# Performance work log

Measured on AMD Instinct MI355X. Metric: run time of the kernel, lower is better.

## Reference

```python
import jax, jax.numpy as jnp
import numpy as np

NEG_SLOPE = 0.2


def _gat_layer(x, src, dst, W, att_s, att_d, bias):
    # x: [N, F_in]; W: [F_in, H*C]; att_s/att_d: [H, C]; bias: [H*C]
    N = x.shape[0]
    H, C = att_s.shape
    h = (x @ W).reshape(N, H, C)                      # projected features [N,H,C]
    a_src = jnp.einsum('nhc,hc->nh', h, att_s)        # [N,H] per-node src logits
    a_dst = jnp.einsum('nhc,hc->nh', h, att_d)        # [N,H]
    e = a_src[src] + a_dst[dst]                       # [E,H] edge logits
    e = jnp.where(e > 0, e, NEG_SLOPE * e)            # leaky_relu
    # scatter-softmax over incoming edges of each destination node
    m = jax.ops.segment_max(e, dst, num_segments=N)   # [N,H]
    ex = jnp.exp(e - m[dst])                          # [E,H]
    denom = jax.ops.segment_sum(ex, dst, num_segments=N)  # [N,H]
    alpha = ex / denom[dst]                           # [E,H]
    # scatter-add aggregation of weighted source features
    msg = h[src] * alpha[:, :, None]                  # [E,H,C]
    out = jax.ops.segment_sum(msg, dst, num_segments=N)   # [N,H,C]
    return out.reshape(N, H * C) + bias


def _with_self_loops(edge_index, N):
    loop = jnp.arange(N, dtype=edge_index.dtype)
    src = jnp.concatenate([edge_index[0], loop])
    dst = jnp.concatenate([edge_index[1], loop])
    return src, dst


def setup_inputs() -> dict:
    key = jax.random.key(0)
    ks = jax.random.split(key, 10)
    N, E = 50000, 800000
    F_in, C1, H1, F_out = 128, 64, 4, 128
    x = jax.random.normal(ks[0], (N, F_in), dtype=jnp.float32)
    edge_index = jax.random.randint(ks[1], (2, E), 0, N, dtype=jnp.int64)
    s1 = 1.0 / np.sqrt(F_in)
    W1 = jax.random.normal(ks[2], (F_in, H1 * C1), dtype=jnp.float32) * s1
    att_src1 = jax.random.normal(ks[3], (H1, C1), dtype=jnp.float32) * 0.1
    att_dst1 = jax.random.normal(ks[4], (H1, C1), dtype=jnp.float32) * 0.1
    bias1 = jnp.zeros((H1 * C1,), dtype=jnp.float32)
    s2 = 1.0 / np.sqrt(H1 * C1)
    W2 = jax.random.normal(ks[5], (H1 * C1, F_out), dtype=jnp.float32) * s2
    att_src2 = jax.random.normal(ks[6], (1, F_out), dtype=jnp.float32) * 0.1
    att_dst2 = jax.random.normal(ks[7], (1, F_out), dtype=jnp.float32) * 0.1
    bias2 = jnp.zeros((F_out,), dtype=jnp.float32)
    return {"x": x, "edge_index": edge_index,
            "W1": W1, "att_src1": att_src1, "att_dst1": att_dst1, "bias1": bias1,
            "W2": W2, "att_src2": att_src2, "att_dst2": att_dst2, "bias2": bias2}


def reference(x, edge_index, W1, att_src1, att_dst1, bias1,
              W2, att_src2, att_dst2, bias2):
    N = x.shape[0]
    src, dst = _with_self_loops(edge_index, N)
    h1 = _gat_layer(x, src, dst, W1, att_src1, att_dst1, bias1)
    h1 = jax.nn.elu(h1)
    out = _gat_layer(h1, src, dst, W2, att_src2, att_dst2, bias2)
    return out
```

## Files before the change

kernel.cpp:

```cpp
#include <hip/hip_runtime.h>

#define NN 50000
#define NE 800000

constexpr int H1 = 4, F1 = 128, HC1 = 256;
constexpr int HC2 = 128;
constexpr int GM1 = (NN + 63) / 64;
constexpr int GE  = (NE + 255) / 256;

typedef unsigned short u16;
typedef unsigned int u32;
typedef __attribute__((ext_vector_type(8))) short bf16x8;
typedef __attribute__((ext_vector_type(4))) float f32x4;

__device__ __forceinline__ float bf2f(u16 h) {
    return __uint_as_float(((u32)h) << 16);
}
__device__ __forceinline__ u16 f2bf(float f) {
    u32 u = __float_as_uint(f);
    u32 r = (u + 0x7fffu + ((u >> 16) & 1u)) >> 16;
    return (u16)r;
}

__device__ __forceinline__ int ld_edge(const int* e32, const long long* e64, int is64, long long idx) {
    return is64 ? (int)e64[idx] : e32[idx];
}

__global__ __launch_bounds__(256) void k_prep(
    const float* __restrict__ x, const float* __restrict__ W1, const float* __restrict__ W2,
    u16* __restrict__ xb, u16* __restrict__ wp1, u16* __restrict__ wp2,
    int* __restrict__ deg, const int* __restrict__ e32, int* __restrict__ flag)
{
    const int b = blockIdx.x, tid = threadIdx.x;
    if (b < 3125) {
        int i = b * 256 + tid;
        const float4* p = (const float4*)x + (size_t)i * 2;
        float4 a = p[0], c = p[1];
        ushort4 o0, o1;
        o0.x = f2bf(a.x); o0.y = f2bf(a.y); o0.z = f2bf(a.z); o0.w = f2bf(a.w);
        o1.x = f2bf(c.x); o1.y = f2bf(c.y); o1.z = f2bf(c.z); o1.w = f2bf(c.w);
        ((ushort4*)xb)[(size_t)i * 2] = o0;
        ((ushort4*)xb)[(size_t)i * 2 + 1] = o1;
    } else if (b < 3253) {
        int o = (b - 3125) * 256 + tid;
        int j = o & 7, lk = (o >> 3) & 3, nn = (o >> 5) & 255, kc = o >> 13;
        int k = kc * 32 + lk * 8 + j;
        wp1[o] = f2bf(W1[(size_t)k * HC1 + nn]);
    } else if (b < 3381) {
        int o = (b - 3253) * 256 + tid;
        int j = o & 7, lk = (o >> 3) & 3, nn = (o >> 5) & 127, kc = o >> 12;
        int k = kc * 32 + lk * 8 + j;
        wp2[o] = f2bf(W2[(size_t)k * HC2 + nn]);
    } else {
        int i = (b - 3381) * 256 + tid;
        if (i < NN) deg[i] = 0;
        if (b == 3381 && tid == 0) {
            int z = 1;
            for (int t = 0; t < 16; t++)
                if (e32[2 * t + 1] != 0) z = 0;
            *flag = z;
        }
    }
}

__global__ void k_count(const int* __restrict__ e32, const long long* __restrict__ e64,
                        const int* __restrict__ flag, int* __restrict__ deg) {
    int e = blockIdx.x * blockDim.x + threadIdx.x;
    if (e >= NE) return;
    int is64 = *flag;
    int dst = ld_edge(e32, e64, is64, (long long)NE + e);
    atomicAdd(&deg[dst], 1);
}

__global__ __launch_bounds__(256) void k_part(const int* __restrict__ deg, int* __restrict__ bsum) {
    int i = blockIdx.x * 256 + threadIdx.x;
    int v = (i < NN) ? deg[i] : 0;
    #pragma unroll
    for (int off = 1; off < 64; off <<= 1) v += __shfl_xor(v, off);
    __shared__ int ws[4];
    if ((threadIdx.x & 63) == 0) ws[threadIdx.x >> 6] = v;
    __syncthreads();
    if (threadIdx.x == 0) bsum[blockIdx.x] = ws[0] + ws[1] + ws[2] + ws[3];
}

__global__ __launch_bounds__(256) void k_scanb(const int* __restrict__ bsum, int* __restrict__ boff,
                                               int* __restrict__ row_ptr, int NB) {
    const int tid = threadIdx.x;
    const int lane = tid & 63, wv = tid >> 6;
    int v = (tid < NB) ? bsum[tid] : 0;
    int x = v;
    #pragma unroll
    for (int off = 1; off < 64; off <<= 1) {
        int t = __shfl_up(x, off);
        if (lane >= off) x += t;
    }
    __shared__ int wsum[4], woff[4];
    if (lane == 63) wsum[wv] = x;
    __syncthreads();
    if (tid == 0) {
        int run = 0;
        #pragma unroll
        for (int j = 0; j < 4; j++) { woff[j] = run; run += wsum[j]; }
        row_ptr[NN] = run;
    }
    __syncthreads();
    if (tid < NB) boff[tid] = x - v + woff[wv];
}

__global__ __launch_bounds__(256) void k_addb(const int* __restrict__ deg, const int* __restrict__ boff,
                                              int* __restrict__ row_ptr, int* __restrict__ cursor) {
    const int tid = threadIdx.x;
    const int lane = tid & 63, wv = tid >> 6;
    int i = blockIdx.x * 256 + tid;
    int v = (i < NN) ? deg[i] : 0;
    int x = v;
    #pragma unroll
    for (int off = 1; off < 64; off <<= 1) {
        int t = __shfl_up(x, off);
        if (lane >= off) x += t;
    }
    __shared__ int wsum[4], woff[4];
    if (lane == 63) wsum[wv] = x;
    __syncthreads();
    if (tid == 0) {
        int run = 0;
        #pragma unroll
        for (int j = 0; j < 4; j++) { woff[j] = run; run += wsum[j]; }
    }
    __syncthreads();
    int excl = x - v + woff[wv] + boff[blockIdx.x];
    if (i < NN) { row_ptr[i] = excl; cursor[i] = excl; }
}

__global__ void k_fill(const int* __restrict__ e32, const long long* __restrict__ e64,
                       const int* __restrict__ flag, int* __restrict__ cursor, int* __restrict__ col) {
    int e = blockIdx.x * blockDim.x + threadIdx.x;
    if (e >= NE) return;
    int is64 = *flag;
    int src = ld_edge(e32, e64, is64, e);
    int dst = ld_edge(e32, e64, is64, (long long)NE + e);
    int pos = atomicAdd(&cursor[dst], 1);
    col[pos] = src;
}

template <int K, int NOUT, int HEADS, int TPB>
__device__ __forceinline__ void gemm_body(
    int bid, const u16* __restrict__ Ab, const u16* __restrict__ Wp,
    const float* __restrict__ atts, const float* __restrict__ attd,
    u16* __restrict__ Hout, float* __restrict__ as_out, float* __restrict__ ad_out, int M)
{
    constexpr int BM = 64, BK = 32;
    constexpr int NK = K / BK;
    constexpr int C = NOUT / HEADS;
    constexpr int LDA = 40;
    __shared__ __align__(16) u16 As[2][BM * LDA];
    __shared__ float red_s[BM * HEADS];
    __shared__ float red_d[BM * HEADS];

    const int tid = threadIdx.x;
    const int w = tid >> 6;
    const int l = tid & 63;
    const int l15 = l & 15, lk = l >> 4;
    const int row0 = bid * BM;
    const int col0 = w * 64;

    for (int i = tid; i < BM * HEADS; i += TPB) { red_s[i] = 0.f; red_d[i] = 0.f; }

    f32x4 acc[4][4];
    #pragma unroll
    for (int rt = 0; rt < 4; rt++)
        #pragma unroll
        for (int nt = 0; nt < 4; nt++)
            acc[rt][nt] = (f32x4){0.f, 0.f, 0.f, 0.f};

    auto stage = [&](int kc, int b) {
        #pragma unroll
        for (int i = tid; i < BM * 4; i += TPB) {
            int r = i >> 2, c = (i & 3) * 8;
            int gr = row0 + r;
            bf16x8 v = {0, 0, 0, 0, 0, 0, 0, 0};
            if (gr < M) v = *(const bf16x8*)(Ab + (size_t)gr * K + kc * BK + c);
            *(bf16x8*)&As[b][r * LDA + c] = v;
        }
    };
    auto loadB = [&](int kc, bf16x8* bf) {
        #pragma unroll
        for (int nt = 0; nt < 4; nt++)
            bf[nt] = *(const bf16x8*)(Wp + (((size_t)kc * NOUT + col0 + nt * 16 + l15) * 4 + lk) * 8);
    };

    bf16x8 bcur[4];
    loadB(0, bcur);
    stage(0, 0);
    for (int kc = 0; kc < NK; ++kc) {
        __syncthreads();
        bf16x8 afr[4];
        #pragma unroll
        for (int rt = 0; rt < 4; rt++)
            afr[rt] = *(const bf16x8*)&As[kc & 1][(rt * 16 + l15) * LDA + lk * 8];
        bf16x8 bnext[4];
        if (kc + 1 < NK) {
            loadB(kc + 1, bnext);
            stage(kc + 1, (kc + 1) & 1);
        }
        #pragma unroll
        for (int rt = 0; rt < 4; rt++)
            #pragma unroll
            for (int nt = 0; nt < 4; nt++)
                acc[rt][nt] = __builtin_amdgcn_mfma_f32_16x16x32_bf16(afr[rt], bcur[nt], acc[rt][nt], 0, 0, 0);
        if (kc + 1 < NK) {
            #pragma unroll
            for (int nt = 0; nt < 4; nt++) bcur[nt] = bnext[nt];
        }
    }

    #pragma unroll
    for (int rt = 0; rt < 4; rt++) {
        #pragma unroll
        for (int t = 0; t < 4; t++) {
            int gr = row0 + rt * 16 + lk * 4 + t;
            if (gr < M) {
                #pragma unroll
                for (int nt = 0; nt < 4; nt++)
                    Hout[(size_t)gr * NOUT + col0 + nt * 16 + l15] = f2bf(acc[rt][nt][t]);
            }
        }
    }

    float avs[4], avd[4];
    #pragma unroll
    for (int nt = 0; nt < 4; nt++) {
        int gc = col0 + nt * 16 + l15;
        avs[nt] = atts[gc];
        avd[nt] = attd[gc];
    }
    const int headw = col0 / C;
    #pragma unroll
    for (int rt = 0; rt < 4; rt++) {
        #pragma unroll
        for (int t = 0; t < 4; t++) {
            float ps = 0.f, pd = 0.f;
            #pragma unroll
            for (int nt = 0; nt < 4; nt++) {
                ps = fmaf(acc[rt][nt][t], avs[nt], ps);
                pd = fmaf(acc[rt][nt][t], avd[nt], pd);
            }
            ps += __shfl_xor(ps, 1); ps += __shfl_xor(ps, 2);
            ps += __shfl_xor(ps, 4); ps += __shfl_xor(ps, 8);
            pd += __shfl_xor(pd, 1); pd += __shfl_xor(pd, 2);
            pd += __shfl_xor(pd, 4); pd += __shfl_xor(pd, 8);
            if (l15 == 0) {
                int row = rt * 16 + lk * 4 + t;
                atomicAdd(&red_s[row * HEADS + headw], ps);
                atomicAdd(&red_d[row * HEADS + headw], pd);
            }
        }
    }
    __syncthreads();
    for (int i = tid; i < BM * HEADS; i += TPB) {
        int gr = row0 + i / HEADS;
        if (gr < M) {
            as_out[(size_t)gr * HEADS + i % HEADS] = red_s[i];
            ad_out[(size_t)gr * HEADS + i % HEADS] = red_d[i];
        }
    }
}

template <int K, int NOUT, int HEADS, int TPB>
__global__ __launch_bounds__(TPB) void k_gemm_mfma(
    const u16* __restrict__ Ab, const u16* __restrict__ Wp,
    const float* __restrict__ atts, const float* __restrict__ attd,
    u16* __restrict__ Hout, float* __restrict__ as_out, float* __restrict__ ad_out, int M)
{
    gemm_body<K, NOUT, HEADS, TPB>(blockIdx.x, Ab, Wp, atts, attd, Hout, as_out, ad_out, M);
}

__global__ __launch_bounds__(256) void k_agg1(
    const int* __restrict__ row_ptr, const int* __restrict__ col,
    const u16* __restrict__ Hb, const float* __restrict__ as_, const float* __restrict__ ad_,
    const float* __restrict__ bias, u16* __restrict__ outp)
{
    __shared__ int    s_src[4][64];
    __shared__ float4 s_p[4][64];
    int n = blockIdx.x * 4 + (threadIdx.x >> 6);
    const int lane = threadIdx.x & 63;
    const int wv = threadIdx.x >> 6;
    const int half = lane >> 5, l32 = lane & 31;
    const int head8 = l32 >> 3;
    float4 ad4 = *(const float4*)(ad_ + (size_t)n * 4);
    int beg = row_ptr[n];
    int cnt = row_ptr[n + 1] - beg + 1;
    float4 sp = make_float4(0.f, 0.f, 0.f, 0.f);
    float a0 = 0.f, a1 = 0.f, a2 = 0.f, a3 = 0.f;
    float a4 = 0.f, a5 = 0.f, a6 = 0.f, a7 = 0.f;
    for (int c = 0; c < cnt; c += 64) {
        int idx = c + lane;
        int srcl = n;
        float4 p4 = make_float4(0.f, 0.f, 0.f, 0.f);
        if (idx < cnt) {
            srcl = (idx == 0) ? n : col[beg + idx - 1];
            float4 aa = *(const float4*)(as_ + (size_t)srcl * 4);
            float e;
            e = aa.x + ad4.x; e = e > 0.f ? e : 0.2f * e; p4.x = __expf(e);
            e = aa.y + ad4.y; e = e > 0.f ? e : 0.2f * e; p4.y = __expf(e);
            e = aa.z + ad4.z; e = e > 0.f ? e : 0.2f * e; p4.z = __expf(e);
            e = aa.w + ad4.w; e = e > 0.f ? e : 0.2f * e; p4.w = __expf(e);
        }
        sp.x += p4.x; sp.y += p4.y; sp.z += p4.z; sp.w += p4.w;
        s_src[wv][lane] = srcl;
        s_p[wv][lane] = p4;
        int jmax = min(64, cnt - c);
        #pragma unroll 4
        for (int j = 0; j < jmax; j += 2) {
            int jj = j + half;
            int srcj = s_src[wv][jj];
            float pj = ((const float*)&s_p[wv][jj])[head8];
            bf16x8 hv = *(const bf16x8*)(Hb + (size_t)srcj * HC1 + l32 * 8);
            a0 = fmaf(pj, bf2f((u16)hv[0]), a0);
            a1 = fmaf(pj, bf2f((u16)hv[1]), a1);
            a2 = fmaf(pj, bf2f((u16)hv[2]), a2);
            a3 = fmaf(pj, bf2f((u16)hv[3]), a3);
            a4 = fmaf(pj, bf2f((u16)hv[4]), a4);
            a5 = fmaf(pj, bf2f((u16)hv[5]), a5);
            a6 = fmaf(pj, bf2f((u16)hv[6]), a6);
            a7 = fmaf(pj, bf2f((u16)hv[7]), a7);
        }
    }
    a0 += __shfl_xor(a0, 32); a1 += __shfl_xor(a1, 32);
    a2 += __shfl_xor(a2, 32); a3 += __shfl_xor(a3, 32);
    a4 += __shfl_xor(a4, 32); a5 += __shfl_xor(a5, 32);
    a6 += __shfl_xor(a6, 32); a7 += __shfl_xor(a7, 32);
    #pragma unroll
    for (int off = 1; off < 64; off <<= 1) {
        sp.x += __shfl_xor(sp.x, off);
        sp.y += __shfl_xor(sp.y, off);
        sp.z += __shfl_xor(sp.z, off);
        sp.w += __shfl_xor(sp.w, off);
    }
    if (lane < 32) {
        float s = head8 < 2 ? (head8 == 0 ? sp.x : sp.y) : (head8 == 2 ? sp.z : sp.w);
        float inv = 1.f / s;
        int ch0 = l32 * 8;
        float4 bv0 = *(const float4*)(bias + ch0);
        float4 bv1 = *(const float4*)(bias + ch0 + 4);
        float o0 = a0 * inv + bv0.x, o1 = a1 * inv + bv0.y;
        float o2 = a2 * inv + bv0.z, o3 = a3 * inv + bv0.w;
        float o4 = a4 * inv + bv1.x, o5 = a5 * inv + bv1.y;
        float o6 = a6 * inv + bv1.z, o7 = a7 * inv + bv1.w;
        o0 = o0 > 0.f ? o0 : __expf(o0) - 1.f;
        o1 = o1 > 0.f ? o1 : __expf(o1) - 1.f;
        o2 = o2 > 0.f ? o2 : __expf(o2) - 1.f;
        o3 = o3 > 0.f ? o3 : __expf(o3) - 1.f;
        o4 = o4 > 0.f ? o4 : __expf(o4) - 1.f;
        o5 = o5 > 0.f ? o5 : __expf(o5) - 1.f;
        o6 = o6 > 0.f ? o6 : __expf(o6) - 1.f;
        o7 = o7 > 0.f ? o7 : __expf(o7) - 1.f;
        bf16x8 ob;
        ob[0] = (short)f2bf(o0); ob[1] = (short)f2bf(o1);
        ob[2] = (short)f2bf(o2); ob[3] = (short)f2bf(o3);
        ob[4] = (short)f2bf(o4); ob[5] = (short)f2bf(o5);
        ob[6] = (short)f2bf(o6); ob[7] = (short)f2bf(o7);
        *(bf16x8*)(outp + (size_t)n * HC1 + ch0) = ob;
    }
}

__global__ __launch_bounds__(256) void k_agg2(
    const int* __restrict__ row_ptr, const int* __restrict__ col,
    const u16* __restrict__ Hb, const float* __restrict__ as_, const float* __restrict__ ad_,
    const float* __restrict__ bias, float* __restrict__ outp)
{
    __shared__ int   s_src[4][64];
    __shared__ float s_p[4][64];
    int n = blockIdx.x * 4 + (threadIdx.x >> 6);
    const int lane = threadIdx.x & 63;
    const int wv = threadIdx.x >> 6;
    const int half = lane >> 5, l32 = lane & 31;
    float ad0 = ad_[n];
    int beg = row_ptr[n];
    int cnt = row_ptr[n + 1] - beg + 1;
    float sp = 0.f;
    float a0 = 0.f, a1 = 0.f, a2 = 0.f, a3 = 0.f;
    for (int c = 0; c < cnt; c += 64) {
        int idx = c + lane;
        int srcl = n;
        float p = 0.f;
        if (idx < cnt) {
            srcl = (idx == 0) ? n : col[beg + idx - 1];
            float e = as_[srcl] + ad0;
            e = e > 0.f ? e : 0.2f * e;
            p = __expf(e);
        }
        sp += p;
        s_src[wv][lane] = srcl;
        s_p[wv][lane] = p;
        int jmax = min(64, cnt - c);
        #pragma unroll 4
        for (int j = 0; j < jmax; j += 2) {
            int jj = j + half;
            int srcj = s_src[wv][jj];
            float pj = s_p[wv][jj];
            ushort4 hv = *(const ushort4*)(Hb + (size_t)srcj * HC2 + l32 * 4);
            a0 = fmaf(pj, bf2f(hv.x), a0);
            a1 = fmaf(pj, bf2f(hv.y), a1);
            a2 = fmaf(pj, bf2f(hv.z), a2);
            a3 = fmaf(pj, bf2f(hv.w), a3);
        }
    }
    a0 += __shfl_xor(a0, 32); a1 += __shfl_xor(a1, 32);
    a2 += __shfl_xor(a2, 32); a3 += __shfl_xor(a3, 32);
    #pragma unroll
    for (int off = 1; off < 64; off <<= 1) sp += __shfl_xor(sp, off);
    if (lane < 32) {
        float inv = 1.f / sp;
        int ch0 = l32 * 4;
        float4 bv = *(const float4*)(bias + ch0);
        float4 o;
        o.x = a0 * inv + bv.x;
        o.y = a1 * inv + bv.y;
        o.z = a2 * inv + bv.z;
        o.w = a3 * inv + bv.w;
        *(float4*)(outp + (size_t)n * HC2 + ch0) = o;
    }
}

extern "C" void kernel_launch(void* const* d_in, const int* in_sizes, int n_in,
                              void* d_out, int out_size, void* d_ws, size_t ws_size,
                              hipStream_t stream) {
    const float* x   = (const float*)d_in[0];
    const int*       e32 = (const int*)d_in[1];
    const long long* e64 = (const long long*)d_in[1];
    const float* W1  = (const float*)d_in[2];
    const float* as1w = (const float*)d_in[3];
    const float* ad1w = (const float*)d_in[4];
    const float* b1  = (const float*)d_in[5];
    const float* W2  = (const float*)d_in[6];
    const float* as2w = (const float*)d_in[7];
    const float* ad2w = (const float*)d_in[8];
    const float* b2  = (const float*)d_in[9];
    float* out = (float*)d_out;

    char* w = (char*)d_ws;
    auto carve = [&](size_t bytes) -> void* {
        void* p = (void*)w;
        w += (bytes + 255) & ~(size_t)255;
        return p;
    };
    int*   flag    = (int*)carve(4);
    int*   row_ptr = (int*)carve((NN + 1) * sizeof(int));
    int*   cursor  = (int*)carve(NN * sizeof(int));
    int*   col     = (int*)carve(NE * sizeof(int));
    int*   bsum    = (int*)carve(256 * sizeof(int));
    int*   boff    = (int*)carve(256 * sizeof(int));
    float* as1     = (float*)carve((size_t)NN * H1 * sizeof(float));
    float* ad1     = (float*)carve((size_t)NN * H1 * sizeof(float));
    float* as2     = (float*)carve((size_t)NN * sizeof(float));
    float* ad2     = (float*)carve((size_t)NN * sizeof(float));
    u16*   xb      = (u16*)carve((size_t)NN * F1 * sizeof(u16));
    u16*   h1b     = (u16*)carve((size_t)NN * HC1 * sizeof(u16));
    u16*   h2in    = (u16*)carve((size_t)NN * HC1 * sizeof(u16));
    u16*   h2b     = (u16*)carve((size_t)NN * HC2 * sizeof(u16));
    u16*   wp1     = (u16*)carve((size_t)F1 * HC1 * sizeof(u16));
    u16*   wp2     = (u16*)carve((size_t)HC1 * HC2 * sizeof(u16));

    const int TPB = 256;
    const int gN  = (NN + TPB - 1) / TPB;
    const int gAgg = NN / 4;

    k_prep<<<3125 + 128 + 128 + 196, 256, 0, stream>>>(x, W1, W2, xb, wp1, wp2, cursor, e32, flag);

    k_count<<<GE, TPB, 0, stream>>>(e32, e64, flag, cursor);
    k_part<<<gN, TPB, 0, stream>>>(cursor, bsum);
    k_scanb<<<1, 256, 0, stream>>>(bsum, boff, row_ptr, gN);
    k_addb<<<gN, TPB, 0, stream>>>(cursor, boff, row_ptr, cursor);
    k_fill<<<GE, TPB, 0, stream>>>(e32, e64, flag, cursor, col);

    k_gemm_mfma<F1, HC1, H1, 256><<<GM1, 256, 0, stream>>>(xb, wp1, as1w, ad1w, h1b, as1, ad1, NN);
    k_agg1<<<gAgg, TPB, 0, stream>>>(row_ptr, col, h1b, as1, ad1, b1, h2in);

    k_gemm_mfma<HC1, HC2, 1, 128><<<GM1, 128, 0, stream>>>(h2in, wp2, as2w, ad2w, h2b, as2, ad2, NN);
    k_agg2<<<gAgg, TPB, 0, stream>>>(row_ptr, col, h2b, as2, ad2, b2, out);
}
```

Measured before the change: 237.3 us.

## Fuse degree counting into prep kernel and remap agg1 to one edge per wave

Degree counting moves into the prep kernel as extra blocks, and the deg array is now zeroed with a memset before launch, which removes one kernel launch. Each count block recomputes the int32/int64 edge-format check inline. Layer-1 aggregation changes its lane mapping: all 64 lanes now process one edge per step and each lane loads 4 bf16 channels, where before each half-wave handled a separate edge with 8 channels. This drops the cross-half shuffle reduction, but each lane issues narrower loads and the inner loop runs twice as many iterations.

```diff
diff --git a/kernel.cpp b/kernel.cpp
--- a/kernel.cpp
+++ b/kernel.cpp
@@ -29,7 +29,8 @@
 __global__ __launch_bounds__(256) void k_prep(
     const float* __restrict__ x, const float* __restrict__ W1, const float* __restrict__ W2,
     u16* __restrict__ xb, u16* __restrict__ wp1, u16* __restrict__ wp2,
-    int* __restrict__ deg, const int* __restrict__ e32, int* __restrict__ flag)
+    int* __restrict__ deg, const int* __restrict__ e32, const long long* __restrict__ e64,
+    int* __restrict__ flag)
 {
     const int b = blockIdx.x, tid = threadIdx.x;
     if (b < 3125) {
@@ -51,25 +52,23 @@
         int j = o & 7, lk = (o >> 3) & 3, nn = (o >> 5) & 127, kc = o >> 12;
         int k = kc * 32 + lk * 8 + j;
         wp2[o] = f2bf(W2[(size_t)k * HC2 + nn]);
-    } else {
-        int i = (b - 3381) * 256 + tid;
-        if (i < NN) deg[i] = 0;
-        if (b == 3381 && tid == 0) {
+    } else if (b == 3381) {
+        if (tid == 0) {
             int z = 1;
             for (int t = 0; t < 16; t++)
                 if (e32[2 * t + 1] != 0) z = 0;
             *flag = z;
         }
-    }
-}
-
-__global__ void k_count(const int* __restrict__ e32, const long long* __restrict__ e64,
-                        const int* __restrict__ flag, int* __restrict__ deg) {
-    int e = blockIdx.x * blockDim.x + threadIdx.x;
-    if (e >= NE) return;
-    int is64 = *flag;
-    int dst = ld_edge(e32, e64, is64, (long long)NE + e);
-    atomicAdd(&deg[dst], 1);
+    } else {
+        int e = (b - 3382) * 256 + tid;
+        if (e < NE) {
+            int z = 1;
+            #pragma unroll
+            for (int t = 0; t < 16; t++) z &= (e32[2 * t + 1] == 0);
+            int dst = z ? (int)e64[(long long)NE + e] : e32[(long long)NE + e];
+            atomicAdd(&deg[dst], 1);
+        }
+    }
 }
 
 __global__ __launch_bounds__(256) void k_part(const int* __restrict__ deg, int* __restrict__ bsum) {
@@ -283,53 +282,43 @@
     __shared__ int    s_src[4][64];
     __shared__ float4 s_p[4][64];
     int n = blockIdx.x * 4 + (threadIdx.x >> 6);
+    if (n >= NN) return;
     const int lane = threadIdx.x & 63;
     const int wv = threadIdx.x >> 6;
-    const int half = lane >> 5, l32 = lane & 31;
-    const int head8 = l32 >> 3;
+    const int head = lane >> 4;
     float4 ad4 = *(const float4*)(ad_ + (size_t)n * 4);
     int beg = row_ptr[n];
     int cnt = row_ptr[n + 1] - beg + 1;
     float4 sp = make_float4(0.f, 0.f, 0.f, 0.f);
-    float a0 = 0.f, a1 = 0.f, a2 = 0.f, a3 = 0.f;
-    float a4 = 0.f, a5 = 0.f, a6 = 0.f, a7 = 0.f;
+    float ax = 0.f, ay = 0.f, az = 0.f, aw = 0.f;
     for (int c = 0; c < cnt; c += 64) {
         int idx = c + lane;
         int srcl = n;
         float4 p4 = make_float4(0.f, 0.f, 0.f, 0.f);
         if (idx < cnt) {
             srcl = (idx == 0) ? n : col[beg + idx - 1];
-            float4 aa = *(const float4*)(as_ + (size_t)srcl * 4);
+            float4 a4 = *(const float4*)(as_ + (size_t)srcl * 4);
             float e;
-            e = aa.x + ad4.x; e = e > 0.f ? e : 0.2f * e; p4.x = __expf(e);
-            e = aa.y + ad4.y; e = e > 0.f ? e : 0.2f * e; p4.y = __expf(e);
-            e = aa.z + ad4.z; e = e > 0.f ? e : 0.2f * e; p4.z = __expf(e);
-            e = aa.w + ad4.w; e = e > 0.f ? e : 0.2f * e; p4.w = __expf(e);
+            e = a4.x + ad4.x; e = e > 0.f ? e : 0.2f * e; p4.x = __expf(e);
+            e = a4.y + ad4.y; e = e > 0.f ? e : 0.2f * e; p4.y = __expf(e);
+            e = a4.z + ad4.z; e = e > 0.f ? e : 0.2f * e; p4.z = __expf(e);
+            e = a4.w + ad4.w; e = e > 0.f ? e : 0.2f * e; p4.w = __expf(e);
         }
         sp.x += p4.x; sp.y += p4.y; sp.z += p4.z; sp.w += p4.w;
         s_src[wv][lane] = srcl;
         s_p[wv][lane] = p4;
         int jmax = min(64, cnt - c);
         #pragma unroll 4
-        for (int j = 0; j < jmax; j += 2) {
-            int jj = j + half;
-            int srcj = s_src[wv][jj];
-            float pj = ((const float*)&s_p[wv][jj])[head8];
-            bf16x8 hv = *(const bf16x8*)(Hb + (size_t)srcj * HC1 + l32 * 8);
-            a0 = fmaf(pj, bf2f((u16)hv[0]), a0);
-            a1 = fmaf(pj, bf2f((u16)hv[1]), a1);
-            a2 = fmaf(pj, bf2f((u16)hv[2]), a2);
-            a3 = fmaf(pj, bf2f((u16)hv[3]), a3);
-            a4 = fmaf(pj, bf2f((u16)hv[4]), a4);
-            a5 = fmaf(pj, bf2f((u16)hv[5]), a5);
-            a6 = fmaf(pj, bf2f((u16)hv[6]), a6);
-            a7 = fmaf(pj, bf2f((u16)hv[7]), a7);
-        }
-    }
-    a0 += __shfl_xor(a0, 32); a1 += __shfl_xor(a1, 32);
-    a2 += __shfl_xor(a2, 32); a3 += __shfl_xor(a3, 32);
-    a4 += __shfl_xor(a4, 32); a5 += __shfl_xor(a5, 32);
-    a6 += __shfl_xor(a6, 32); a7 += __shfl_xor(a7, 32);
+        for (int j = 0; j < jmax; ++j) {
+            int srcj = s_src[wv][j];
+            float pj = ((const float*)&s_p[wv][j])[head];
+            ushort4 hv = *(const ushort4*)(Hb + (size_t)srcj * HC1 + lane * 4);
+            ax = fmaf(pj, bf2f(hv.x), ax);
+            ay = fmaf(pj, bf2f(hv.y), ay);
+            az = fmaf(pj, bf2f(hv.z), az);
+            aw = fmaf(pj, bf2f(hv.w), aw);
+        }
+    }
     #pragma unroll
     for (int off = 1; off < 64; off <<= 1) {
         sp.x += __shfl_xor(sp.x, off);
@@ -337,31 +326,21 @@
         sp.z += __shfl_xor(sp.z, off);
         sp.w += __shfl_xor(sp.w, off);
     }
-    if (lane < 32) {
-        float s = head8 < 2 ? (head8 == 0 ? sp.x : sp.y) : (head8 == 2 ? sp.z : sp.w);
-        float inv = 1.f / s;
-        int ch0 = l32 * 8;
-        float4 bv0 = *(const float4*)(bias + ch0);
-        float4 bv1 = *(const float4*)(bias + ch0 + 4);
-        float o0 = a0 * inv + bv0.x, o1 = a1 * inv + bv0.y;
-        float o2 = a2 * inv + bv0.z, o3 = a3 * inv + bv0.w;
-        float o4 = a4 * inv + bv1.x, o5 = a5 * inv + bv1.y;
-        float o6 = a6 * inv + bv1.z, o7 = a7 * inv + bv1.w;
-        o0 = o0 > 0.f ? o0 : __expf(o0) - 1.f;
-        o1 = o1 > 0.f ? o1 : __expf(o1) - 1.f;
-        o2 = o2 > 0.f ? o2 : __expf(o2) - 1.f;
-        o3 = o3 > 0.f ? o3 : __expf(o3) - 1.f;
-        o4 = o4 > 0.f ? o4 : __expf(o4) - 1.f;
-        o5 = o5 > 0.f ? o5 : __expf(o5) - 1.f;
-        o6 = o6 > 0.f ? o6 : __expf(o6) - 1.f;
-        o7 = o7 > 0.f ? o7 : __expf(o7) - 1.f;
-        bf16x8 ob;
-        ob[0] = (short)f2bf(o0); ob[1] = (short)f2bf(o1);
-        ob[2] = (short)f2bf(o2); ob[3] = (short)f2bf(o3);
-        ob[4] = (short)f2bf(o4); ob[5] = (short)f2bf(o5);
-        ob[6] = (short)f2bf(o6); ob[7] = (short)f2bf(o7);
-        *(bf16x8*)(outp + (size_t)n * HC1 + ch0) = ob;
-    }
+    float s = head < 2 ? (head == 0 ? sp.x : sp.y) : (head == 2 ? sp.z : sp.w);
+    float inv = 1.f / s;
+    float4 bv = *(const float4*)(bias + lane * 4);
+    float4 o;
+    o.x = ax * inv + bv.x;
+    o.y = ay * inv + bv.y;
+    o.z = az * inv + bv.z;
+    o.w = aw * inv + bv.w;
+    o.x = o.x > 0.f ? o.x : __expf(o.x) - 1.f;
+    o.y = o.y > 0.f ? o.y : __expf(o.y) - 1.f;
+    o.z = o.z > 0.f ? o.z : __expf(o.z) - 1.f;
+    o.w = o.w > 0.f ? o.w : __expf(o.w) - 1.f;
+    ushort4 ob;
+    ob.x = f2bf(o.x); ob.y = f2bf(o.y); ob.z = f2bf(o.z); ob.w = f2bf(o.w);
+    *(ushort4*)(outp + (size_t)n * HC1 + lane * 4) = ob;
 }
 
 __global__ __launch_bounds__(256) void k_agg2(
@@ -466,9 +445,10 @@
     const int gN  = (NN + TPB - 1) / TPB;
     const int gAgg = NN / 4;
 
-    k_prep<<<3125 + 128 + 128 + 196, 256, 0, stream>>>(x, W1, W2, xb, wp1, wp2, cursor, e32, flag);
-
-    k_count<<<GE, TPB, 0, stream>>>(e32, e64, flag, cursor);
+    hipMemsetAsync(cursor, 0, NN * sizeof(int), stream);
+
+    k_prep<<<3382 + GE, 256, 0, stream>>>(x, W1, W2, xb, wp1, wp2, cursor, e32, e64, flag);
+
     k_part<<<gN, TPB, 0, stream>>>(cursor, bsum);
     k_scanb<<<1, 256, 0, stream>>>(bsum, boff, row_ptr, gN);
     k_addb<<<gN, TPB, 0, stream>>>(cursor, boff, row_ptr, cursor);
```

Result: no change. 237.1 us (-0.1%).
